# Performance work log

Measured on AMD Instinct MI355X. Metric: run time of the kernel, lower is better.

Reference implementation:

```python
import jax, jax.numpy as jnp
import numpy as np

N_NODES = 714
LRELU = 0.01   # nn.LeakyReLU default
GAT_SLOPE = 0.2  # PyG GATConv internal leaky_relu slope


def _gcn_conv(x, row, col, W, b, n):
    # PyG GCNConv: h = x W; sym-normalized aggregation over edges (self loops already appended)
    h = x @ W
    ones = jnp.ones(row.shape[0], h.dtype)
    deg = jax.ops.segment_sum(ones, col, num_segments=n)
    dinv = jnp.where(deg > 0, jax.lax.rsqrt(deg), 0.0)
    norm = dinv[row] * dinv[col]
    out = jax.ops.segment_sum(h[row] * norm[:, None], col, num_segments=n)
    return out + b


def _gat_conv(x, row, col, W, a_src, a_dst, b, n):
    # PyG GATConv, heads=1: h = x W (no lin bias); edge score = leaky_relu(a_src.h_j + a_dst.h_i)
    h = x @ W
    asrc = h @ a_src
    adst = h @ a_dst
    e = jax.nn.leaky_relu(asrc[row] + adst[col], GAT_SLOPE)
    emax = jax.ops.segment_max(e, col, num_segments=n)
    ee = jnp.exp(e - emax[col])
    denom = jax.ops.segment_sum(ee, col, num_segments=n)
    alpha = ee / (denom[col] + 1e-16)
    out = jax.ops.segment_sum(h[row] * alpha[:, None], col, num_segments=n)
    return out + b


def _forward(feature, edges, poi_tab, cat_tab, lat_tab, long_tab,
             W_in, b_in, gat_W, gat_asrc, gat_adst, gat_b,
             W_out, b_out, W_fc1, b_fc1, W_fc2, b_fc2):
    B, n, _ = feature.shape
    # embedding lookups, concat -> [B, n, 800]
    x = jnp.concatenate([
        poi_tab[feature[..., 0]],
        cat_tab[feature[..., 1]],
        lat_tab[feature[..., 3]],
        long_tab[feature[..., 4]],
    ], axis=-1)
    # append self loops (both GCNConv and GATConv add them by default)
    sl = jnp.arange(n, dtype=edges.dtype)
    sl2 = jnp.broadcast_to(jnp.stack([sl, sl])[None], (B, 2, n))
    ei = jnp.concatenate([edges, sl2], axis=2)  # [B, 2, E+n]
    lrelu = lambda t: jax.nn.leaky_relu(t, LRELU)

    def per_graph(xg, eg):
        row, col = eg[0], eg[1]
        h = lrelu(_gcn_conv(xg, row, col, W_in, b_in, n))
        for i in range(gat_W.shape[0]):  # 3 AGCNUnits, each reuses ONE GATConv twice
            t = _gat_conv(h, row, col, gat_W[i], gat_asrc[i], gat_adst[i], gat_b[i], n)
            h = lrelu(t) + t
            h = lrelu(_gat_conv(h, row, col, gat_W[i], gat_asrc[i], gat_adst[i], gat_b[i], n))
        h = lrelu(_gcn_conv(h, row, col, W_out, b_out, n))  # [n, 1]
        return h[:, 0]

    g = jax.vmap(per_graph)(x, ei)  # [B, n]
    h = jax.nn.leaky_relu(g @ W_fc1 + b_fc1, LRELU)
    return h @ W_fc2 + b_fc2  # [B, 128]


def setup_inputs() -> dict:
    key = jax.random.key(0)
    ks = jax.random.split(key, 20)
    B, E, n = 64, 16384, N_NODES
    C = 128
    feature = jax.random.randint(ks[0], (B, n, 5), 0, 400, dtype=jnp.int64)
    edges = jax.random.randint(ks[1], (B, 2, E), 0, n, dtype=jnp.int64)
    weight = jax.random.normal(ks[2], (B, E, 2), dtype=jnp.float32)
    s = lambda k, shp, fan: (jax.random.normal(k, shp, jnp.float32) / np.sqrt(fan)).astype(jnp.float32)
    return {
        'feature': feature, 'edges': edges, 'weight': weight,
        'poi_tab': s(ks[3], (5099, 300), 1), 'cat_tab': s(ks[4], (400, 100), 1),
        'lat_tab': s(ks[5], (7128, 200), 1), 'long_tab': s(ks[6], (6394, 200), 1),
        'W_in': s(ks[7], (800, C), 800), 'b_in': jnp.zeros((C,), jnp.float32),
        'gat_W': s(ks[8], (3, C, C), C), 'gat_asrc': s(ks[9], (3, C), C),
        'gat_adst': s(ks[10], (3, C), C), 'gat_b': jnp.zeros((3, C), jnp.float32),
        'W_out': s(ks[11], (C, 1), C), 'b_out': jnp.zeros((1,), jnp.float32),
        'W_fc1': s(ks[12], (n, 128), n), 'b_fc1': jnp.zeros((128,), jnp.float32),
        'W_fc2': s(ks[13], (128, 128), 128), 'b_fc2': jnp.zeros((128,), jnp.float32),
    }


def reference(feature, edges, weight, poi_tab, cat_tab, lat_tab, long_tab,
              W_in, b_in, gat_W, gat_asrc, gat_adst, gat_b,
              W_out, b_out, W_fc1, b_fc1, W_fc2, b_fc2):
    # `weight` (edge_attr) is sliced in the original forward but never used in the math
    return _forward(feature, edges, poi_tab, cat_tab, lat_tab, long_tab,
                    W_in, b_in, gat_W, gat_asrc, gat_adst, gat_b,
                    W_out, b_out, W_fc1, b_fc1, W_fc2, b_fc2)
```

## Files before the change

### kernel.cpp

```cpp
#include <hip/hip_runtime.h>


#define BB 64
#define NN 714
#define EE 16384
#define ET (EE + NN)
#define NBt (BB * NN)
#define CC 128
#define RP (NN + 1)
#define DFAST 64
#define KSP 28
#define PROJ_ROWS 19021

typedef _Float16 f16;
typedef __attribute__((ext_vector_type(8))) _Float16 f16x8;
typedef __attribute__((ext_vector_type(4))) _Float16 f16x4;
typedef __attribute__((ext_vector_type(4))) float f32x4;

__device__ __forceinline__ float lrelu01(float x) { return x > 0.f ? x : 0.01f * x; }
__device__ __forceinline__ float lrelu2(float x)  { return x > 0.f ? x : 0.2f  * x; }

__device__ __forceinline__ float wsum(float x) {
#pragma unroll
    for (int o = 32; o > 0; o >>= 1) x += __shfl_xor(x, o);
    return x;
}
__device__ __forceinline__ float hsum(float x) {
#pragma unroll
    for (int o = 16; o > 0; o >>= 1) x += __shfl_xor(x, o);
    return x;
}
__device__ __forceinline__ float hmax(float x) {
#pragma unroll
    for (int o = 16; o > 0; o >>= 1) x = fmaxf(x, __shfl_xor(x, o));
    return x;
}

__device__ __forceinline__ int xcd_swz(int bid, int nwg) {
    int q = nwg >> 3, r = nwg & 7;
    int x = bid & 7, l = bid >> 3;
    int base = (x < r) ? x * (q + 1) : r * (q + 1) + (x - r) * q;
    return base + l;
}

#define NSEG (KSP * 8 * 64)
#define NGAT (3 * 4 * 8 * 64)
#define NPREP (NSEG + NGAT + 3 * CC)
__global__ __launch_bounds__(1024) void k_build_prep(
    const int* __restrict__ edges, int* __restrict__ rowptr,
    int* __restrict__ csr_row, float* __restrict__ dinv,
    const float* __restrict__ W, const float* __restrict__ gat_W,
    const float* __restrict__ a_s, const float* __restrict__ a_d,
    f16* __restrict__ BWh, f16* __restrict__ BWl,
    f16* __restrict__ BGh, f16* __restrict__ BGl,
    float* __restrict__ wsv, float* __restrict__ wdv) {
    __shared__ int degs[NN];
    __shared__ int scan[1024];
    __shared__ int curs[NN];
    int t = threadIdx.x;
    if (blockIdx.x < BB) {
        int b = blockIdx.x;
        if (t < NN) degs[t] = 0;
        __syncthreads();
        int rr[17], cc[17];
#pragma unroll
        for (int q = 0; q < 17; ++q) {
            int e = q * 1024 + t;
            int r = -1, c = -1;
            if (e < ET) {
                if (e < EE) { r = edges[b * 2 * EE + e]; c = edges[b * 2 * EE + EE + e]; }
                else        { r = c = e - EE; }
                atomicAdd(&degs[c], 1);
            }
            rr[q] = r; cc[q] = c;
        }
        __syncthreads();
        int cnt = (t < NN) ? degs[t] : 0;
        scan[t] = cnt;
        __syncthreads();
        for (int off = 1; off < 1024; off <<= 1) {
            int val = (t >= off) ? scan[t - off] : 0;
            __syncthreads();
            scan[t] += val;
            __syncthreads();
        }
        if (t < NN) {
            rowptr[b * RP + t + 1] = scan[t];
            curs[t] = scan[t] - cnt;
            dinv[b * NN + t] = cnt > 0 ? rsqrtf((float)cnt) : 0.f;
        }
        if (t == 0) rowptr[b * RP] = 0;
        __syncthreads();
#pragma unroll
        for (int q = 0; q < 17; ++q) {
            if (cc[q] >= 0) {
                int slot = atomicAdd(&curs[cc[q]], 1);
                csr_row[b * ET + slot] = rr[q];
            }
        }
        return;
    }
    int idx = (blockIdx.x - BB) * 1024 + t;
    if (idx < NSEG) {
        int lane = idx & 63, tc = idx >> 6;
        int ct = tc & 7, ks = tc >> 3;
        int tt = ks < 10 ? 0 : ks < 14 ? 1 : ks < 21 ? 2 : 3;
        int k0 = tt == 0 ? 0 : tt == 1 ? 10 : tt == 2 ? 14 : 21;
        const int Ktab[4] = {300, 100, 200, 200};
        const int Koff[4] = {0, 300, 400, 600};
        int ksl = ks - k0;
        f16x8 ph, pl;
#pragma unroll
        for (int j = 0; j < 8; ++j) {
            int k = ksl * 32 + (lane >> 4) * 8 + j;
            int c = ct * 16 + (lane & 15);
            float v = (k < Ktab[tt]) ? W[(size_t)(Koff[tt] + k) * CC + c] : 0.f;
            f16 hi = (f16)v;
            ph[j] = hi; pl[j] = (f16)(v - (float)hi);
        }
        *(f16x8*)(BWh + (size_t)idx * 8) = ph;
        *(f16x8*)(BWl + (size_t)idx * 8) = pl;
    } else if (idx < NSEG + NGAT) {
        int i2 = idx - NSEG;
        int lane = i2 & 63, tc = i2 >> 6;
        int ct = tc & 7; tc >>= 3;
        int ks = tc & 3, li = tc >> 2;
        const float* Wl = gat_W + (size_t)li * CC * CC;
        f16x8 ph, pl;
#pragma unroll
        for (int j = 0; j < 8; ++j) {
            int k = ks * 32 + (lane >> 4) * 8 + j;
            int c = ct * 16 + (lane & 15);
            float v = Wl[k * CC + c];
            f16 hi = (f16)v;
            ph[j] = hi; pl[j] = (f16)(v - (float)hi);
        }
        *(f16x8*)(BGh + (size_t)i2 * 8) = ph;
        *(f16x8*)(BGl + (size_t)i2 * 8) = pl;
    } else if (idx < NPREP) {
        int i2 = idx - NSEG - NGAT;
        int i = i2 >> 7, k = i2 & 127;
        const float* Wl = gat_W + (size_t)i * CC * CC;
        float s = 0.f, d = 0.f;
#pragma unroll 4
        for (int c = 0; c < CC; ++c) {
            float w = Wl[k * CC + c];
            s = fmaf(w, a_s[i * CC + c], s);
            d = fmaf(w, a_d[i * CC + c], d);
        }
        wsv[i * CC + k] = s; wdv[i * CC + k] = d;
    }
}

__global__ __launch_bounds__(256) void k_proj(
    const float* __restrict__ poi, const float* __restrict__ cat,
    const float* __restrict__ lat, const float* __restrict__ lon,
    const f16* __restrict__ Bh, const f16* __restrict__ Bl,
    float* __restrict__ P) {
    int bid = blockIdx.x;
    int t, r0;
    if (bid < 160)      { t = 0; r0 = bid * 32; }
    else if (bid < 173) { t = 1; r0 = (bid - 160) * 32; }
    else if (bid < 396) { t = 2; r0 = (bid - 173) * 32; }
    else                { t = 3; r0 = (bid - 396) * 32; }
    const int Ktab[4] = {300, 100, 200, 200};
    const int Rtab[4] = {5099, 400, 7128, 6394};
    const int Rofs[4] = {0, 5099, 5499, 12627};
    const int Kst[4]  = {10, 4, 7, 7};
    const int Bks0[4] = {0, 10, 14, 21};
    const float* tab = t == 0 ? poi : t == 1 ? cat : t == 2 ? lat : lon;
    int K = Ktab[t], R = Rtab[t], nks = Kst[t], bks = Bks0[t];
    int lane = threadIdx.x & 63, w = threadIdx.x >> 6;
    int ct0 = w * 2;
    f32x4 acc[2][2];
#pragma unroll
    for (int rt = 0; rt < 2; ++rt)
#pragma unroll
        for (int c = 0; c < 2; ++c) acc[rt][c] = (f32x4){0.f, 0.f, 0.f, 0.f};

    for (int ks = 0; ks < nks; ++ks) {
        int kbase = ks * 32 + (lane >> 4) * 8;
        f16x8 ah[2], al[2];
#pragma unroll
        for (int rt = 0; rt < 2; ++rt) {
            int row = r0 + rt * 16 + (lane & 15);
            int rowc = row < R ? row : R - 1;
            const float* rp = tab + (size_t)rowc * K;
            float v[8];
            if (kbase + 8 <= K) {
                float4 x0 = ((const float4*)(rp + kbase))[0];
                float4 x1 = ((const float4*)(rp + kbase))[1];
                v[0] = x0.x; v[1] = x0.y; v[2] = x0.z; v[3] = x0.w;
                v[4] = x1.x; v[5] = x1.y; v[6] = x1.z; v[7] = x1.w;
            } else if (kbase >= K) {
#pragma unroll
                for (int m = 0; m < 8; ++m) v[m] = 0.f;
            } else {
#pragma unroll
                for (int m = 0; m < 8; ++m) v[m] = (kbase + m < K) ? rp[kbase + m] : 0.f;
            }
#pragma unroll
            for (int j = 0; j < 8; ++j) {
                f16 hi = (f16)v[j];
                ah[rt][j] = hi; al[rt][j] = (f16)(v[j] - (float)hi);
            }
        }
#pragma unroll
        for (int cti = 0; cti < 2; ++cti) {
            int ct = ct0 + cti;
            f16x8 bh = *(const f16x8*)(Bh + ((size_t)((bks + ks) * 8 + ct) * 64 + lane) * 8);
            f16x8 bl = *(const f16x8*)(Bl + ((size_t)((bks + ks) * 8 + ct) * 64 + lane) * 8);
#pragma unroll
            for (int rt = 0; rt < 2; ++rt) {
                acc[rt][cti] = __builtin_amdgcn_mfma_f32_16x16x32_f16(ah[rt], bh, acc[rt][cti], 0, 0, 0);
                acc[rt][cti] = __builtin_amdgcn_mfma_f32_16x16x32_f16(al[rt], bh, acc[rt][cti], 0, 0, 0);
                acc[rt][cti] = __builtin_amdgcn_mfma_f32_16x16x32_f16(ah[rt], bl, acc[rt][cti], 0, 0, 0);
            }
        }
    }
#pragma unroll
    for (int rt = 0; rt < 2; ++rt)
#pragma unroll
        for (int cti = 0; cti < 2; ++cti)
#pragma unroll
            for (int i = 0; i < 4; ++i) {
                int row = r0 + rt * 16 + (lane >> 4) * 4 + i;
                if (row < R) {
                    int col = (ct0 + cti) * 16 + (lane & 15);
                    P[(size_t)(Rofs[t] + row) * CC + col] = acc[rt][cti][i];
                }
            }
}

__global__ __launch_bounds__(256) void k_assemble(
    const int* __restrict__ feature, const float* __restrict__ P,
    f16* __restrict__ out) {
    int tid = xcd_swz(blockIdx.x, gridDim.x) * 256 + threadIdx.x;
    int g = tid >> 4, c8 = (tid & 15) * 8;
    const int* f = feature + (size_t)g * 5;
    const float4* p0 = (const float4*)(P + (size_t)f[0] * CC + c8);
    const float4* p1 = (const float4*)(P + (size_t)(5099 + f[1]) * CC + c8);
    const float4* p2 = (const float4*)(P + (size_t)(5499 + f[3]) * CC + c8);
    const float4* p3 = (const float4*)(P + (size_t)(12627 + f[4]) * CC + c8);
    float4 a0 = p0[0], a1 = p0[1];
    float4 b0 = p1[0], b1 = p1[1];
    float4 c0 = p2[0], c1 = p2[1];
    float4 d0 = p3[0], d1 = p3[1];
    f16x8 r;
    r[0] = (f16)(a0.x + b0.x + c0.x + d0.x);
    r[1] = (f16)(a0.y + b0.y + c0.y + d0.y);
    r[2] = (f16)(a0.z + b0.z + c0.z + d0.z);
    r[3] = (f16)(a0.w + b0.w + c0.w + d0.w);
    r[4] = (f16)(a1.x + b1.x + c1.x + d1.x);
    r[5] = (f16)(a1.y + b1.y + c1.y + d1.y);
    r[6] = (f16)(a1.z + b1.z + c1.z + d1.z);
    r[7] = (f16)(a1.w + b1.w + c1.w + d1.w);
    *(f16x8*)(out + (size_t)g * CC + c8) = r;
}

__global__ __launch_bounds__(256) void k_gat_gemm(
    const f16* __restrict__ hin, const f16* __restrict__ Bh, const f16* __restrict__ Bl,
    const float* __restrict__ wsv, const float* __restrict__ wdv,
    f16* __restrict__ Hp, float* __restrict__ asrc, float* __restrict__ adst) {
    __shared__ __align__(16) f16 Ah[32 * 128];
    __shared__ float reds[256], redd[256];
    int t = threadIdx.x;
    int g0 = xcd_swz(blockIdx.x, gridDim.x) * 32;
    int lane = t & 63, w = t >> 6;
    int sr = t >> 3, skb = (t & 7) * 16;
    const f16x8* hrow = (const f16x8*)(hin + (size_t)(g0 + sr) * CC + skb);
    f16x8 hv0 = hrow[0], hv1 = hrow[1];
    float ps = 0.f, pd = 0.f;
#pragma unroll
    for (int m = 0; m < 8; ++m) {
        ps = fmaf((float)hv0[m], wsv[skb + m], ps);
        pd = fmaf((float)hv0[m], wdv[skb + m], pd);
        ps = fmaf((float)hv1[m], wsv[skb + 8 + m], ps);
        pd = fmaf((float)hv1[m], wdv[skb + 8 + m], pd);
    }
    {
        int kg0 = (t & 7) * 2;
        int ad0 = sr * 128 + ((kg0 ^ (sr & 7)) << 3);
        int ad1 = sr * 128 + (((kg0 + 1) ^ (sr & 7)) << 3);
        *(f16x8*)&Ah[ad0] = hv0;
        *(f16x8*)&Ah[ad1] = hv1;
    }
    reds[t] = ps; redd[t] = pd;
    __syncthreads();
    if (t < 32) {
        float s = 0.f, d = 0.f;
#pragma unroll
        for (int q = 0; q < 8; ++q) { s += reds[t * 8 + q]; d += redd[t * 8 + q]; }
        asrc[g0 + t] = s; adst[g0 + t] = d;
    }
    f32x4 acc[2][2];
#pragma unroll
    for (int rt = 0; rt < 2; ++rt)
#pragma unroll
        for (int c = 0; c < 2; ++c) acc[rt][c] = (f32x4){0.f, 0.f, 0.f, 0.f};
    int ct0 = w * 2;
#pragma unroll
    for (int ks = 0; ks < 4; ++ks) {
        f16x8 ahf[2];
#pragma unroll
        for (int rt = 0; rt < 2; ++rt) {
            int r = rt * 16 + (lane & 15);
            int kg = (lane >> 4) + ks * 4;
            int ad = r * 128 + ((kg ^ (r & 7)) << 3);
            ahf[rt] = *(const f16x8*)&Ah[ad];
        }
#pragma unroll
        for (int cti = 0; cti < 2; ++cti) {
            int ct = ct0 + cti;
            f16x8 bh = *(const f16x8*)(Bh + ((size_t)(ks * 8 + ct) * 64 + lane) * 8);
            f16x8 bl = *(const f16x8*)(Bl + ((size_t)(ks * 8 + ct) * 64 + lane) * 8);
#pragma unroll
            for (int rt = 0; rt < 2; ++rt) {
                acc[rt][cti] = __builtin_amdgcn_mfma_f32_16x16x32_f16(ahf[rt], bh, acc[rt][cti], 0, 0, 0);
                acc[rt][cti] = __builtin_amdgcn_mfma_f32_16x16x32_f16(ahf[rt], bl, acc[rt][cti], 0, 0, 0);
            }
        }
    }
#pragma unroll
    for (int rt = 0; rt < 2; ++rt)
#pragma unroll
        for (int cti = 0; cti < 2; ++cti)
#pragma unroll
            for (int i = 0; i < 4; ++i) {
                int row = g0 + rt * 16 + (lane >> 4) * 4 + i;
                int col = (ct0 + cti) * 16 + (lane & 15);
                Hp[(size_t)row * CC + col] = (f16)acc[rt][cti][i];
            }
}

template <int MODE>
__global__ __launch_bounds__(256) void k_agg(
    const f16* __restrict__ Hp, const float* __restrict__ aux,
    const float* __restrict__ adst, const int* __restrict__ rowptr,
    const int* __restrict__ csr_row, const float* __restrict__ bias,
    f16* __restrict__ out, const float* __restrict__ Wout, float* __restrict__ pscal) {
    __shared__ float2 pr[4][2][DFAST];
    int wid = threadIdx.x >> 6, lane = threadIdx.x & 63;
    int half = lane >> 5, hl = lane & 31;
    int g = xcd_swz(blockIdx.x, gridDim.x) * 8 + wid * 2 + half;
    int b = g / NN, v = g - b * NN;
    int bN = b * NN, bE = b * ET;
    int s0 = rowptr[b * RP + v], s1 = rowptr[b * RP + v + 1];
    int deg = s1 - s0;

    if (deg <= DFAST) {
        int degp = (deg + 7) & ~7;
        float inv = 1.f;
        int r0 = 0, r1 = 0;
        float w0, w1;
        if (MODE == 2) {
            float dv = aux[g];
            w0 = w1 = 0.f;
            if (hl < deg)      { r0 = csr_row[bE + s0 + hl];      w0 = aux[bN + r0] * dv; }
            if (hl + 32 < deg) { r1 = csr_row[bE + s0 + hl + 32]; w1 = aux[bN + r1] * dv; }
        } else {
            float adv = adst[g];
            float e0 = -3.0e38f, e1 = -3.0e38f;
            if (hl < deg)      { r0 = csr_row[bE + s0 + hl];      e0 = lrelu2(aux[bN + r0] + adv); }
            if (hl + 32 < deg) { r1 = csr_row[bE + s0 + hl + 32]; e1 = lrelu2(aux[bN + r1] + adv); }
            float m = hmax(fmaxf(e0, e1));
            w0 = __expf(e0 - m);
            w1 = __expf(e1 - m);
            float ss = hsum(w0 + w1);
            inv = 1.f / (ss + 1e-16f);
        }
        if (hl < degp)      pr[wid][half][hl]      = make_float2(w0, __int_as_float(r0));
        if (hl + 32 < degp) pr[wid][half][hl + 32] = make_float2(w1, __int_as_float(r1));
        int eh = hl >> 4, ql = hl & 15;
        const f16* Hb = Hp + (size_t)bN * CC;
        float acc0[8], acc1[8], acc2[8], acc3[8];
#pragma unroll
        for (int j = 0; j < 8; ++j) { acc0[j] = 0.f; acc1[j] = 0.f; acc2[j] = 0.f; acc3[j] = 0.f; }
        for (int jj = 0; jj < degp; jj += 8) {
            float2 p0 = pr[wid][half][jj + eh];
            float2 p1 = pr[wid][half][jj + 2 + eh];
            float2 p2 = pr[wid][half][jj + 4 + eh];
            float2 p3 = pr[wid][half][jj + 6 + eh];
            f16x8 h0 = *(const f16x8*)(Hb + (size_t)__float_as_int(p0.y) * CC + ql * 8);
            f16x8 h1 = *(const f16x8*)(Hb + (size_t)__float_as_int(p1.y) * CC + ql * 8);
            f16x8 h2 = *(const f16x8*)(Hb + (size_t)__float_as_int(p2.y) * CC + ql * 8);
            f16x8 h3 = *(const f16x8*)(Hb + (size_t)__float_as_int(p3.y) * CC + ql * 8);
#pragma unroll
            for (int j = 0; j < 8; ++j) {
                acc0[j] = fmaf((float)h0[j], p0.x, acc0[j]);
                acc1[j] = fmaf((float)h1[j], p1.x, acc1[j]);
                acc2[j] = fmaf((float)h2[j], p2.x, acc2[j]);
                acc3[j] = fmaf((float)h3[j], p3.x, acc3[j]);
            }
        }
        float a0[8];
#pragma unroll
        for (int j = 0; j < 8; ++j) {
            float x = acc0[j] + acc1[j] + acc2[j] + acc3[j];
            x += __shfl_xor(x, 16);
            a0[j] = x;
        }
        if (eh == 0) {
            float sc = (MODE == 2) ? 1.f : inv;
            float4 bb0 = ((const float4*)bias)[ql * 2];
            float4 bb1 = ((const float4*)bias)[ql * 2 + 1];
            float tv[8];
            tv[0] = a0[0] * sc + bb0.x; tv[1] = a0[1] * sc + bb0.y;
            tv[2] = a0[2] * sc + bb0.z; tv[3] = a0[3] * sc + bb0.w;
            tv[4] = a0[4] * sc + bb1.x; tv[5] = a0[5] * sc + bb1.y;
            tv[6] = a0[6] * sc + bb1.z; tv[7] = a0[7] * sc + bb1.w;
            float ov[8];
#pragma unroll
            for (int j = 0; j < 8; ++j) {
                float l = lrelu01(tv[j]);
                ov[j] = (MODE == 0) ? l + tv[j] : l;
            }
            if (MODE == 3) {
                float4 w0v = ((const float4*)Wout)[ql * 2];
                float4 w1v = ((const float4*)Wout)[ql * 2 + 1];
                float p = ov[0] * w0v.x + ov[1] * w0v.y + ov[2] * w0v.z + ov[3] * w0v.w
                        + ov[4] * w1v.x + ov[5] * w1v.y + ov[6] * w1v.z + ov[7] * w1v.w;
#pragma unroll
                for (int o = 8; o > 0; o >>= 1) p += __shfl_xor(p, o);
                if (ql == 0) pscal[g] = p;
            } else {
                f16x8 r;
#pragma unroll
                for (int j = 0; j < 8; ++j) r[j] = (f16)ov[j];
                *(f16x8*)(out + (size_t)g * CC + ql * 8) = r;
            }
        }
        return;
    }
    {
        float wsc0 = 0.f;
        float m = 0.f, inv = 1.f, adv = 0.f;
        if (MODE != 2) {
            adv = adst[g];
            m = -3.0e38f;
            for (int j = s0 + hl; j < s1; j += 32)
                m = fmaxf(m, lrelu2(aux[bN + csr_row[bE + j]] + adv));
            m = hmax(m);
            float ssum = 0.f;
            for (int j = s0 + hl; j < s1; j += 32)
                ssum += __expf(lrelu2(aux[bN + csr_row[bE + j]] + adv) - m);
            ssum = hsum(ssum);
            inv = 1.f / (ssum + 1e-16f);
        } else {
            wsc0 = aux[g];
        }
        float x0 = 0.f, x1 = 0.f, x2 = 0.f, x3 = 0.f;
        for (int j = s0; j < s1; ++j) {
            int r = csr_row[bE + j];
            float wj = (MODE == 2) ? aux[bN + r]
                                   : __expf(lrelu2(aux[bN + r] + adv) - m) * inv;
            f16x4 h = *(const f16x4*)(Hp + (size_t)(bN + r) * CC + hl * 4);
            x0 = fmaf(wj, (float)h[0], x0);
            x1 = fmaf(wj, (float)h[1], x1);
            x2 = fmaf(wj, (float)h[2], x2);
            x3 = fmaf(wj, (float)h[3], x3);
        }
        if (MODE == 2) { x0 *= wsc0; x1 *= wsc0; x2 *= wsc0; x3 *= wsc0; }
        float4 bb = ((const float4*)bias)[hl];
        float t0 = x0 + bb.x, t1 = x1 + bb.y, t2 = x2 + bb.z, t3 = x3 + bb.w;
        float l0 = lrelu01(t0), l1 = lrelu01(t1), l2 = lrelu01(t2), l3 = lrelu01(t3);
        float o0 = (MODE == 0) ? l0 + t0 : l0;
        float o1 = (MODE == 0) ? l1 + t1 : l1;
        float o2 = (MODE == 0) ? l2 + t2 : l2;
        float o3 = (MODE == 0) ? l3 + t3 : l3;
        if (MODE == 3) {
            float4 w4 = ((const float4*)Wout)[hl];
            float p = o0 * w4.x + o1 * w4.y + o2 * w4.z + o3 * w4.w;
            p = hsum(p);
            if (hl == 0) pscal[g] = p;
        } else {
            f16x4 r;
            r[0] = (f16)o0; r[1] = (f16)o1; r[2] = (f16)o2; r[3] = (f16)o3;
            *(f16x4*)(out + (size_t)g * CC + hl * 4) = r;
        }
    }
}

__global__ __launch_bounds__(256) void k_out_agg(
    const float* __restrict__ p, const float* __restrict__ dinv,
    const int* __restrict__ rowptr, const int* __restrict__ csr_row,
    const float* __restrict__ bout, float* __restrict__ gv) {
    int wid = threadIdx.x >> 6, lane = threadIdx.x & 63;
    int g = xcd_swz(blockIdx.x, gridDim.x) * 4 + wid;
    int b = g / NN, v = g - b * NN;
    int s0 = rowptr[b * RP + v], s1 = rowptr[b * RP + v + 1];
    float acc = 0.f;
    for (int j = s0 + lane; j < s1; j += 64) {
        int r = csr_row[b * ET + j];
        acc += dinv[b * NN + r] * p[b * NN + r];
    }
    acc = wsum(acc);
    if (lane == 0) gv[g] = lrelu01(acc * dinv[g] + bout[0]);
}

__global__ __launch_bounds__(128) void k_fc(
    const float* __restrict__ gv, const float* __restrict__ W1,
    const float* __restrict__ b1, const float* __restrict__ W2,
    const float* __restrict__ b2, float* __restrict__ outp) {
    __shared__ float gs[NN];
    __shared__ float s1[CC];
    int b = blockIdx.x, tx = threadIdx.x;
    for (int v = tx; v < NN; v += 128) gs[v] = gv[b * NN + v];
    __syncthreads();
    float acc = 0.f;
    for (int v = 0; v < NN; ++v) acc = fmaf(gs[v], W1[v * CC + tx], acc);
    float t = lrelu01(acc + b1[tx]);
    s1[tx] = t;
    __syncthreads();
    float acc2 = 0.f;
#pragma unroll
    for (int k = 0; k < CC; ++k) acc2 = fmaf(s1[k], W2[k * CC + tx], acc2);
    outp[b * CC + tx] = acc2 + b2[tx];
}

extern "C" void kernel_launch(void* const* d_in, const int* in_sizes, int n_in,
                              void* d_out, int out_size, void* d_ws, size_t ws_size,
                              hipStream_t stream) {
    const int*   feature  = (const int*)d_in[0];
    const int*   edges    = (const int*)d_in[1];
    const float* poi      = (const float*)d_in[3];
    const float* cat      = (const float*)d_in[4];
    const float* lat      = (const float*)d_in[5];
    const float* lon      = (const float*)d_in[6];
    const float* W_in     = (const float*)d_in[7];
    const float* b_in     = (const float*)d_in[8];
    const float* gat_W    = (const float*)d_in[9];
    const float* gat_asrc = (const float*)d_in[10];
    const float* gat_adst = (const float*)d_in[11];
    const float* gat_b    = (const float*)d_in[12];
    const float* W_out    = (const float*)d_in[13];
    const float* b_out    = (const float*)d_in[14];
    const float* W_fc1    = (const float*)d_in[15];
    const float* b_fc1    = (const float*)d_in[16];
    const float* W_fc2    = (const float*)d_in[17];
    const float* b_fc2    = (const float*)d_in[18];
    float* outp = (float*)d_out;

    char* ws = (char*)d_ws;
    size_t off = 0;
    auto take = [&](size_t bytes) -> char* {
        char* pp = ws + off;
        off = (off + bytes + 255) & ~(size_t)255;
        return pp;
    };
    int*   csr    = (int*)take((size_t)BB * ET * 4);
    int*   rowptr = (int*)take((size_t)BB * RP * 4);
    float* dinv   = (float*)take((size_t)NBt * 4);
    float* asrc   = (float*)take((size_t)NBt * 4);
    float* adst   = (float*)take((size_t)NBt * 4);
    float* pscal  = (float*)take((size_t)NBt * 4);
    float* gvec   = (float*)take((size_t)NBt * 4);
    f16*   bufA   = (f16*)take((size_t)NBt * CC * 2);
    f16*   bufB   = (f16*)take((size_t)NBt * CC * 2);
    float* P      = (float*)take((size_t)PROJ_ROWS * CC * 4);
    f16*   BWh    = (f16*)take((size_t)KSP * 8 * 64 * 8 * 2);
    f16*   BWl    = (f16*)take((size_t)KSP * 8 * 64 * 8 * 2);
    f16*   BGh    = (f16*)take((size_t)3 * 4 * 8 * 64 * 8 * 2);
    f16*   BGl    = (f16*)take((size_t)3 * 4 * 8 * 64 * 8 * 2);
    float* wsv    = (float*)take((size_t)3 * CC * 4);
    float* wdv    = (float*)take((size_t)3 * CC * 4);

    const int prep_blocks = (NPREP + 1023) / 1024;
    k_build_prep<<<BB + prep_blocks, 1024, 0, stream>>>(
        edges, rowptr, csr, dinv,
        W_in, gat_W, gat_asrc, gat_adst, BWh, BWl, BGh, BGl, wsv, wdv);

    k_proj<<<596, 256, 0, stream>>>(poi, cat, lat, lon, BWh, BWl, P);
    k_assemble<<<NBt * 16 / 256, 256, 0, stream>>>(feature, P, bufB);
    k_agg<2><<<NBt / 8, 256, 0, stream>>>(bufB, dinv, nullptr, rowptr, csr, b_in,
                                          bufA, nullptr, nullptr);

    for (int i = 0; i < 3; ++i) {
        const f16* bh = BGh + (size_t)i * 4 * 8 * 64 * 8;
        const f16* bl = BGl + (size_t)i * 4 * 8 * 64 * 8;
        const float* ws_i = wsv + (size_t)i * CC;
        const float* wd_i = wdv + (size_t)i * CC;
        const float* gb = gat_b + (size_t)i * CC;
        k_gat_gemm<<<NBt / 32, 256, 0, stream>>>(bufA, bh, bl, ws_i, wd_i, bufB, asrc, adst);
        k_agg<0><<<NBt / 8, 256, 0, stream>>>(bufB, asrc, adst, rowptr, csr, gb,
                                              bufA, nullptr, nullptr);
        k_gat_gemm<<<NBt / 32, 256, 0, stream>>>(bufA, bh, bl, ws_i, wd_i, bufB, asrc, adst);
        if (i < 2) {
            k_agg<1><<<NBt / 8, 256, 0, stream>>>(bufB, asrc, adst, rowptr, csr, gb,
                                                  bufA, nullptr, nullptr);
        } else {
            k_agg<3><<<NBt / 8, 256, 0, stream>>>(bufB, asrc, adst, rowptr, csr, gb,
                                                  bufA, W_out, pscal);
        }
    }

    k_out_agg<<<NBt / 4, 256, 0, stream>>>(pscal, dinv, rowptr, csr, b_out, gvec);
    k_fc<<<BB, 128, 0, stream>>>(gvec, W_fc1, b_fc1, W_fc2, b_fc2, outp);
}
```

Measured before the change: 291.2 us.

## Assign one node per 16-lane quarter-wave in GAT/GCN aggregation kernels

The aggregation kernels now process four destination nodes per wavefront, one per 16-lane group, instead of two per half-wave. Each lane owns 8 channels and walks all of its node's edges sequentially, which removes the cross-half shuffle reduction and halves the grid size. The output aggregation kernel likewise moves from one node per wave to one per quarter-wave. In exchange, each node gets fewer lanes for its edge loads, so per-node latency may rise for high-degree nodes, and the padded shared memory rows grow.

New measurement: 273.6 us (median of 2 runs). -6.0%, faster.

```diff
diff --git a/kernel.cpp b/kernel.cpp
--- a/kernel.cpp
+++ b/kernel.cpp
@@ -25,14 +25,14 @@
     for (int o = 32; o > 0; o >>= 1) x += __shfl_xor(x, o);
     return x;
 }
-__device__ __forceinline__ float hsum(float x) {
-#pragma unroll
-    for (int o = 16; o > 0; o >>= 1) x += __shfl_xor(x, o);
+__device__ __forceinline__ float qsum(float x) {
+#pragma unroll
+    for (int o = 8; o > 0; o >>= 1) x += __shfl_xor(x, o);
     return x;
 }
-__device__ __forceinline__ float hmax(float x) {
-#pragma unroll
-    for (int o = 16; o > 0; o >>= 1) x = fmaxf(x, __shfl_xor(x, o));
+__device__ __forceinline__ float qmax(float x) {
+#pragma unroll
+    for (int o = 8; o > 0; o >>= 1) x = fmaxf(x, __shfl_xor(x, o));
     return x;
 }
 
@@ -339,48 +339,61 @@
     const float* __restrict__ adst, const int* __restrict__ rowptr,
     const int* __restrict__ csr_row, const float* __restrict__ bias,
     f16* __restrict__ out, const float* __restrict__ Wout, float* __restrict__ pscal) {
-    __shared__ float2 pr[4][2][DFAST];
+    __shared__ float2 pr[4][4][DFAST + 2];
     int wid = threadIdx.x >> 6, lane = threadIdx.x & 63;
-    int half = lane >> 5, hl = lane & 31;
-    int g = xcd_swz(blockIdx.x, gridDim.x) * 8 + wid * 2 + half;
+    int quarter = lane >> 4, ql = lane & 15;
+    int g = xcd_swz(blockIdx.x, gridDim.x) * 16 + wid * 4 + quarter;
     int b = g / NN, v = g - b * NN;
     int bN = b * NN, bE = b * ET;
     int s0 = rowptr[b * RP + v], s1 = rowptr[b * RP + v + 1];
     int deg = s1 - s0;
 
     if (deg <= DFAST) {
-        int degp = (deg + 7) & ~7;
+        int degp = (deg + 3) & ~3;
         float inv = 1.f;
-        int r0 = 0, r1 = 0;
-        float w0, w1;
+        int rv[4];
+        float wv[4];
         if (MODE == 2) {
             float dv = aux[g];
-            w0 = w1 = 0.f;
-            if (hl < deg)      { r0 = csr_row[bE + s0 + hl];      w0 = aux[bN + r0] * dv; }
-            if (hl + 32 < deg) { r1 = csr_row[bE + s0 + hl + 32]; w1 = aux[bN + r1] * dv; }
+#pragma unroll
+            for (int u = 0; u < 4; ++u) {
+                int jj = ql + u * 16;
+                rv[u] = 0; wv[u] = 0.f;
+                if (jj < deg) { rv[u] = csr_row[bE + s0 + jj]; wv[u] = aux[bN + rv[u]] * dv; }
+            }
         } else {
             float adv = adst[g];
-            float e0 = -3.0e38f, e1 = -3.0e38f;
-            if (hl < deg)      { r0 = csr_row[bE + s0 + hl];      e0 = lrelu2(aux[bN + r0] + adv); }
-            if (hl + 32 < deg) { r1 = csr_row[bE + s0 + hl + 32]; e1 = lrelu2(aux[bN + r1] + adv); }
-            float m = hmax(fmaxf(e0, e1));
-            w0 = __expf(e0 - m);
-            w1 = __expf(e1 - m);
-            float ss = hsum(w0 + w1);
+            float ev[4];
+#pragma unroll
+            for (int u = 0; u < 4; ++u) {
+                int jj = ql + u * 16;
+                rv[u] = 0; ev[u] = -3.0e38f;
+                if (jj < deg) { rv[u] = csr_row[bE + s0 + jj]; ev[u] = lrelu2(aux[bN + rv[u]] + adv); }
+            }
+            float m = qmax(fmaxf(fmaxf(ev[0], ev[1]), fmaxf(ev[2], ev[3])));
+            float ss = 0.f;
+#pragma unroll
+            for (int u = 0; u < 4; ++u) {
+                wv[u] = __expf(ev[u] - m);
+                ss += wv[u];
+            }
+            ss = qsum(ss);
             inv = 1.f / (ss + 1e-16f);
         }
-        if (hl < degp)      pr[wid][half][hl]      = make_float2(w0, __int_as_float(r0));
-        if (hl + 32 < degp) pr[wid][half][hl + 32] = make_float2(w1, __int_as_float(r1));
-        int eh = hl >> 4, ql = hl & 15;
+#pragma unroll
+        for (int u = 0; u < 4; ++u) {
+            int jj = ql + u * 16;
+            if (jj < degp) pr[wid][quarter][jj] = make_float2(wv[u], __int_as_float(rv[u]));
+        }
         const f16* Hb = Hp + (size_t)bN * CC;
         float acc0[8], acc1[8], acc2[8], acc3[8];
 #pragma unroll
         for (int j = 0; j < 8; ++j) { acc0[j] = 0.f; acc1[j] = 0.f; acc2[j] = 0.f; acc3[j] = 0.f; }
-        for (int jj = 0; jj < degp; jj += 8) {
-            float2 p0 = pr[wid][half][jj + eh];
-            float2 p1 = pr[wid][half][jj + 2 + eh];
-            float2 p2 = pr[wid][half][jj + 4 + eh];
-            float2 p3 = pr[wid][half][jj + 6 + eh];
+        for (int jj = 0; jj < degp; jj += 4) {
+            float2 p0 = pr[wid][quarter][jj];
+            float2 p1 = pr[wid][quarter][jj + 1];
+            float2 p2 = pr[wid][quarter][jj + 2];
+            float2 p3 = pr[wid][quarter][jj + 3];
             f16x8 h0 = *(const f16x8*)(Hb + (size_t)__float_as_int(p0.y) * CC + ql * 8);
             f16x8 h1 = *(const f16x8*)(Hb + (size_t)__float_as_int(p1.y) * CC + ql * 8);
             f16x8 h2 = *(const f16x8*)(Hb + (size_t)__float_as_int(p2.y) * CC + ql * 8);
@@ -393,42 +406,30 @@
                 acc3[j] = fmaf((float)h3[j], p3.x, acc3[j]);
             }
         }
-        float a0[8];
+        float sc = (MODE == 2) ? 1.f : inv;
+        float4 bb0 = ((const float4*)bias)[ql * 2];
+        float4 bb1 = ((const float4*)bias)[ql * 2 + 1];
+        float tv[8], ov[8];
 #pragma unroll
         for (int j = 0; j < 8; ++j) {
             float x = acc0[j] + acc1[j] + acc2[j] + acc3[j];
-            x += __shfl_xor(x, 16);
-            a0[j] = x;
-        }
-        if (eh == 0) {
-            float sc = (MODE == 2) ? 1.f : inv;
-            float4 bb0 = ((const float4*)bias)[ql * 2];
-            float4 bb1 = ((const float4*)bias)[ql * 2 + 1];
-            float tv[8];
-            tv[0] = a0[0] * sc + bb0.x; tv[1] = a0[1] * sc + bb0.y;
-            tv[2] = a0[2] * sc + bb0.z; tv[3] = a0[3] * sc + bb0.w;
-            tv[4] = a0[4] * sc + bb1.x; tv[5] = a0[5] * sc + bb1.y;
-            tv[6] = a0[6] * sc + bb1.z; tv[7] = a0[7] * sc + bb1.w;
-            float ov[8];
-#pragma unroll
-            for (int j = 0; j < 8; ++j) {
-                float l = lrelu01(tv[j]);
-                ov[j] = (MODE == 0) ? l + tv[j] : l;
-            }
-            if (MODE == 3) {
-                float4 w0v = ((const float4*)Wout)[ql * 2];
-                float4 w1v = ((const float4*)Wout)[ql * 2 + 1];
-                float p = ov[0] * w0v.x + ov[1] * w0v.y + ov[2] * w0v.z + ov[3] * w0v.w
-                        + ov[4] * w1v.x + ov[5] * w1v.y + ov[6] * w1v.z + ov[7] * w1v.w;
-#pragma unroll
-                for (int o = 8; o > 0; o >>= 1) p += __shfl_xor(p, o);
-                if (ql == 0) pscal[g] = p;
-            } else {
-                f16x8 r;
-#pragma unroll
-                for (int j = 0; j < 8; ++j) r[j] = (f16)ov[j];
-                *(f16x8*)(out + (size_t)g * CC + ql * 8) = r;
-            }
+            float bv = (j < 4) ? ((const float*)&bb0)[j] : ((const float*)&bb1)[j - 4];
+            tv[j] = x * sc + bv;
+            float l = lrelu01(tv[j]);
+            ov[j] = (MODE == 0) ? l + tv[j] : l;
+        }
+        if (MODE == 3) {
+            float4 w0v = ((const float4*)Wout)[ql * 2];
+            float4 w1v = ((const float4*)Wout)[ql * 2 + 1];
+            float p = ov[0] * w0v.x + ov[1] * w0v.y + ov[2] * w0v.z + ov[3] * w0v.w
+                    + ov[4] * w1v.x + ov[5] * w1v.y + ov[6] * w1v.z + ov[7] * w1v.w;
+            p = qsum(p);
+            if (ql == 0) pscal[g] = p;
+        } else {
+            f16x8 r;
+#pragma unroll
+            for (int j = 0; j < 8; ++j) r[j] = (f16)ov[j];
+            *(f16x8*)(out + (size_t)g * CC + ql * 8) = r;
         }
         return;
     }
@@ -438,45 +439,54 @@
         if (MODE != 2) {
             adv = adst[g];
             m = -3.0e38f;
-            for (int j = s0 + hl; j < s1; j += 32)
+            for (int j = s0 + ql; j < s1; j += 16)
                 m = fmaxf(m, lrelu2(aux[bN + csr_row[bE + j]] + adv));
-            m = hmax(m);
+            m = qmax(m);
             float ssum = 0.f;
-            for (int j = s0 + hl; j < s1; j += 32)
+            for (int j = s0 + ql; j < s1; j += 16)
                 ssum += __expf(lrelu2(aux[bN + csr_row[bE + j]] + adv) - m);
-            ssum = hsum(ssum);
+            ssum = qsum(ssum);
             inv = 1.f / (ssum + 1e-16f);
         } else {
             wsc0 = aux[g];
         }
-        float x0 = 0.f, x1 = 0.f, x2 = 0.f, x3 = 0.f;
+        float acc[8];
+#pragma unroll
+        for (int j = 0; j < 8; ++j) acc[j] = 0.f;
         for (int j = s0; j < s1; ++j) {
             int r = csr_row[bE + j];
             float wj = (MODE == 2) ? aux[bN + r]
                                    : __expf(lrelu2(aux[bN + r] + adv) - m) * inv;
-            f16x4 h = *(const f16x4*)(Hp + (size_t)(bN + r) * CC + hl * 4);
-            x0 = fmaf(wj, (float)h[0], x0);
-            x1 = fmaf(wj, (float)h[1], x1);
-            x2 = fmaf(wj, (float)h[2], x2);
-            x3 = fmaf(wj, (float)h[3], x3);
-        }
-        if (MODE == 2) { x0 *= wsc0; x1 *= wsc0; x2 *= wsc0; x3 *= wsc0; }
-        float4 bb = ((const float4*)bias)[hl];
-        float t0 = x0 + bb.x, t1 = x1 + bb.y, t2 = x2 + bb.z, t3 = x3 + bb.w;
-        float l0 = lrelu01(t0), l1 = lrelu01(t1), l2 = lrelu01(t2), l3 = lrelu01(t3);
-        float o0 = (MODE == 0) ? l0 + t0 : l0;
-        float o1 = (MODE == 0) ? l1 + t1 : l1;
-        float o2 = (MODE == 0) ? l2 + t2 : l2;
-        float o3 = (MODE == 0) ? l3 + t3 : l3;
+            f16x8 h = *(const f16x8*)(Hp + (size_t)(bN + r) * CC + ql * 8);
+#pragma unroll
+            for (int k = 0; k < 8; ++k) acc[k] = fmaf(wj, (float)h[k], acc[k]);
+        }
+        if (MODE == 2) {
+#pragma unroll
+            for (int k = 0; k < 8; ++k) acc[k] *= wsc0;
+        }
+        float4 bb0 = ((const float4*)bias)[ql * 2];
+        float4 bb1 = ((const float4*)bias)[ql * 2 + 1];
+        float ov[8];
+#pragma unroll
+        for (int j = 0; j < 8; ++j) {
+            float bv = (j < 4) ? ((const float*)&bb0)[j] : ((const float*)&bb1)[j - 4];
+            float tvj = acc[j] + bv;
+            float l = lrelu01(tvj);
+            ov[j] = (MODE == 0) ? l + tvj : l;
+        }
         if (MODE == 3) {
-            float4 w4 = ((const float4*)Wout)[hl];
-            float p = o0 * w4.x + o1 * w4.y + o2 * w4.z + o3 * w4.w;
-            p = hsum(p);
-            if (hl == 0) pscal[g] = p;
+            float4 w0v = ((const float4*)Wout)[ql * 2];
+            float4 w1v = ((const float4*)Wout)[ql * 2 + 1];
+            float p = ov[0] * w0v.x + ov[1] * w0v.y + ov[2] * w0v.z + ov[3] * w0v.w
+                    + ov[4] * w1v.x + ov[5] * w1v.y + ov[6] * w1v.z + ov[7] * w1v.w;
+            p = qsum(p);
+            if (ql == 0) pscal[g] = p;
         } else {
-            f16x4 r;
-            r[0] = (f16)o0; r[1] = (f16)o1; r[2] = (f16)o2; r[3] = (f16)o3;
-            *(f16x4*)(out + (size_t)g * CC + hl * 4) = r;
+            f16x8 r;
+#pragma unroll
+            for (int j = 0; j < 8; ++j) r[j] = (f16)ov[j];
+            *(f16x8*)(out + (size_t)g * CC + ql * 8) = r;
         }
     }
 }
@@ -486,16 +496,17 @@
     const int* __restrict__ rowptr, const int* __restrict__ csr_row,
     const float* __restrict__ bout, float* __restrict__ gv) {
     int wid = threadIdx.x >> 6, lane = threadIdx.x & 63;
-    int g = xcd_swz(blockIdx.x, gridDim.x) * 4 + wid;
+    int quarter = lane >> 4, ql = lane & 15;
+    int g = xcd_swz(blockIdx.x, gridDim.x) * 16 + wid * 4 + quarter;
     int b = g / NN, v = g - b * NN;
     int s0 = rowptr[b * RP + v], s1 = rowptr[b * RP + v + 1];
     float acc = 0.f;
-    for (int j = s0 + lane; j < s1; j += 64) {
+    for (int j = s0 + ql; j < s1; j += 16) {
         int r = csr_row[b * ET + j];
         acc += dinv[b * NN + r] * p[b * NN + r];
     }
-    acc = wsum(acc);
-    if (lane == 0) gv[g] = lrelu01(acc * dinv[g] + bout[0]);
+    acc = qsum(acc);
+    if (ql == 0) gv[g] = lrelu01(acc * dinv[g] + bout[0]);
 }
 
 __global__ __launch_bounds__(128) void k_fc(
@@ -572,8 +583,8 @@
 
     k_proj<<<596, 256, 0, stream>>>(poi, cat, lat, lon, BWh, BWl, P);
     k_assemble<<<NBt * 16 / 256, 256, 0, stream>>>(feature, P, bufB);
-    k_agg<2><<<NBt / 8, 256, 0, stream>>>(bufB, dinv, nullptr, rowptr, csr, b_in,
-                                          bufA, nullptr, nullptr);
+    k_agg<2><<<NBt / 16, 256, 0, stream>>>(bufB, dinv, nullptr, rowptr, csr, b_in,
+                                           bufA, nullptr, nullptr);
 
     for (int i = 0; i < 3; ++i) {
         const f16* bh = BGh + (size_t)i * 4 * 8 * 64 * 8;
@@ -582,18 +593,18 @@
         const float* wd_i = wdv + (size_t)i * CC;
         const float* gb = gat_b + (size_t)i * CC;
         k_gat_gemm<<<NBt / 32, 256, 0, stream>>>(bufA, bh, bl, ws_i, wd_i, bufB, asrc, adst);
-        k_agg<0><<<NBt / 8, 256, 0, stream>>>(bufB, asrc, adst, rowptr, csr, gb,
-                                              bufA, nullptr, nullptr);
+        k_agg<0><<<NBt / 16, 256, 0, stream>>>(bufB, asrc, adst, rowptr, csr, gb,
+                                               bufA, nullptr, nullptr);
         k_gat_gemm<<<NBt / 32, 256, 0, stream>>>(bufA, bh, bl, ws_i, wd_i, bufB, asrc, adst);
         if (i < 2) {
-            k_agg<1><<<NBt / 8, 256, 0, stream>>>(bufB, asrc, adst, rowptr, csr, gb,
-                                                  bufA, nullptr, nullptr);
+            k_agg<1><<<NBt / 16, 256, 0, stream>>>(bufB, asrc, adst, rowptr, csr, gb,
+                                                   bufA, nullptr, nullptr);
         } else {
-            k_agg<3><<<NBt / 8, 256, 0, stream>>>(bufB, asrc, adst, rowptr, csr, gb,
-                                                  bufA, W_out, pscal);
-        }
-    }
-
-    k_out_agg<<<NBt / 4, 256, 0, stream>>>(pscal, dinv, rowptr, csr, b_out, gvec);
+            k_agg<3><<<NBt / 16, 256, 0, stream>>>(bufB, asrc, adst, rowptr, csr, gb,
+                                                   bufA, W_out, pscal);
+        }
+    }
+
+    k_out_agg<<<NBt / 16, 256, 0, stream>>>(pscal, dinv, rowptr, csr, b_out, gvec);
     k_fc<<<BB, 128, 0, stream>>>(gvec, W_fc1, b_fc1, W_fc2, b_fc2, outp);
 }
```
